# Performance work log

Hardware: AMD Instinct MI355X
Metric: run time of the kernel (lower is better)

The kernel has to match this reference:

```python
import jax, jax.numpy as jnp
import numpy as np

LENGTH = 100
EMBED = 64
BATCH = 8192


def setup_inputs() -> dict:
    key = jax.random.key(0)
    k1, k2 = jax.random.split(key)
    x = jax.random.normal(k1, (BATCH, LENGTH), dtype=jnp.float32)
    # learned embedding table (nn.Embedding weight)
    W = jax.random.normal(k2, (LENGTH, EMBED), dtype=jnp.float32)
    return {"x": x, "W": W}


def reference(x, W):
    # Torch module computes: result[b, 0, i*E + j] = x[b, i] * W[i, j]
    # (the sparse selector matmul `x @ trans` merely repeats each x column E times,
    #  and the tiled embedding lookup flattens W per batch row).
    B, L = x.shape
    E = W.shape[1]
    out = x[:, :, None] * W[None, :, :]          # [B, L, E]
    return out.reshape(B, 1, L * E)
```

## Files before the change

### kernel.cpp

```cpp
#include <hip/hip_runtime.h>
#include <hip/hip_bf16.h>


#define LENGTH 100
#define EMBED 64
#define BATCH 8192
#define VEC4_PER_ROW (LENGTH * EMBED / 4)

__global__ __launch_bounds__(256) void chemical_embedding_kernel(
    const float* __restrict__ x,
    const float* __restrict__ W,
    float4* __restrict__ out)
{
    int v = blockIdx.x * blockDim.x + threadIdx.x;
    int b = v / VEC4_PER_ROW;
    int r = v - b * VEC4_PER_ROW;
    int i = r >> 4;

    float xs = x[b * LENGTH + i];
    float4 w = reinterpret_cast<const float4*>(W)[r];

    float4 o;
    o.x = xs * w.x;
    o.y = xs * w.y;
    o.z = xs * w.z;
    o.w = xs * w.w;
    out[v] = o;
}

extern "C" void kernel_launch(void* const* d_in, const int* in_sizes, int n_in,
                              void* d_out, int out_size, void* d_ws, size_t ws_size,
                              hipStream_t stream) {
    const float* x = (const float*)d_in[0];
    const float* W = (const float*)d_in[1];
    float4* out = (float4*)d_out;

    const int total_vec4 = BATCH * VEC4_PER_ROW;
    const int block = 256;
    const int grid = total_vec4 / block;

    chemical_embedding_kernel<<<grid, block, 0, stream>>>(x, W, out);
}
```

Measured before the change: 214.2 us.

## Map one block per batch row with multi-vec4 loop and nontemporal stores

Restructures the launch so each 320-thread block handles one batch row and loops over five float4 chunks, removing the per-thread integer division and cutting the block count. Output writes use nontemporal stores so the large write-only output stream does not pollute the caches. The cost is fewer, longer-lived blocks and less latency hiding per thread if the loop does not overlap loads well.

```diff
diff --git a/kernel.cpp b/kernel.cpp
--- a/kernel.cpp
+++ b/kernel.cpp
@@ -5,27 +5,31 @@
 #define LENGTH 100
 #define EMBED 64
 #define BATCH 8192
-#define VEC4_PER_ROW (LENGTH * EMBED / 4)
+#define V4_PER_ROW (LENGTH * EMBED / 4)
+#define TPB 320
 
-__global__ __launch_bounds__(256) void chemical_embedding_kernel(
+typedef float vfloat4 __attribute__((ext_vector_type(4)));
+
+__global__ __launch_bounds__(TPB) void chemical_embedding_kernel(
     const float* __restrict__ x,
     const float* __restrict__ W,
-    float4* __restrict__ out)
+    float* __restrict__ out)
 {
-    int v = blockIdx.x * blockDim.x + threadIdx.x;
-    int b = v / VEC4_PER_ROW;
-    int r = v - b * VEC4_PER_ROW;
-    int i = r >> 4;
+    const int b = blockIdx.x;
+    const int t = threadIdx.x;
 
-    float xs = x[b * LENGTH + i];
-    float4 w = reinterpret_cast<const float4*>(W)[r];
+    const vfloat4* __restrict__ W4 = reinterpret_cast<const vfloat4*>(W);
+    const float*   __restrict__ xrow = x + b * LENGTH;
+    vfloat4*       __restrict__ orow = reinterpret_cast<vfloat4*>(out) + b * V4_PER_ROW;
 
-    float4 o;
-    o.x = xs * w.x;
-    o.y = xs * w.y;
-    o.z = xs * w.z;
-    o.w = xs * w.w;
-    out[v] = o;
+#pragma unroll
+    for (int k = 0; k < V4_PER_ROW / TPB; ++k) {
+        const int r = k * TPB + t;
+        const float s = xrow[r >> 4];
+        vfloat4 w = W4[r];
+        vfloat4 o = s * w;
+        __builtin_nontemporal_store(o, &orow[r]);
+    }
 }
 
 extern "C" void kernel_launch(void* const* d_in, const int* in_sizes, int n_in,
@@ -33,11 +37,7 @@
                               hipStream_t stream) {
     const float* x = (const float*)d_in[0];
     const float* W = (const float*)d_in[1];
-    float4* out = (float4*)d_out;
+    float* out = (float*)d_out;
 
-    const int total_vec4 = BATCH * VEC4_PER_ROW;
-    const int block = 256;
-    const int grid = total_vec4 / block;
-
-    chemical_embedding_kernel<<<grid, block, 0, stream>>>(x, W, out);
+    chemical_embedding_kernel<<<BATCH, TPB, 0, stream>>>(x, W, out);
 }
```

Measured after the change: 222.4 us. 3.9% more time.
